# Performance work log

Measured on AMD Instinct MI355X. Metric: run time of the kernel, lower is better.

The kernel has to match this reference:

```python
import jax, jax.numpy as jnp
import numpy as np

BATCH_SIZE = 8388608            # arg_dict['batch_size']
REG_FACTORS = (0.01, 0.001)     # regular_factor_list
LOG_CLAMP = -100.0              # torch BCELoss clamps log outputs at -100


def setup_inputs() -> dict:
    key = jax.random.key(0)
    k1, k2, k3, k4 = jax.random.split(key, 4)
    B = BATCH_SIZE
    model_outputs = jax.random.uniform(k1, (B,), dtype=jnp.float32)
    labels = jax.random.uniform(k2, (B,), dtype=jnp.float32)
    # weight tensors of the regularized sub-modules (e.g. two Linear layers)
    w1 = jax.random.normal(k3, (4096, 4096), dtype=jnp.float32) * 0.02
    w2 = jax.random.normal(k4, (4096, 1024), dtype=jnp.float32) * 0.02
    return {"model_outputs": model_outputs, "labels": labels, "w1": w1, "w2": w2}


def reference(model_outputs, labels, w1, w2):
    p = model_outputs.reshape(labels.shape)
    # BCE with torch-style log clamping (log clamped to >= -100)
    log_p = jnp.clip(jnp.log(p), LOG_CLAMP)
    log_1mp = jnp.clip(jnp.log1p(-p), LOG_CLAMP)
    cross_loss = -jnp.mean(labels * log_p + (1.0 - labels) * log_1mp)
    # L2 regularization: sum(factor * ||w||^2 / (2 * batch_size))
    reg = (REG_FACTORS[0] * jnp.sum(w1 * w1) / (2.0 * BATCH_SIZE)
           + REG_FACTORS[1] * jnp.sum(w2 * w2) / (2.0 * BATCH_SIZE))
    result = cross_loss + reg
    # vectorized replacement of the per-sample python accuracy loop
    correct_count = jnp.sum(jnp.abs(p - labels) < 0.5)
    return result, correct_count
```

## Files before the change

### kernel.cpp

```cpp
#include <hip/hip_runtime.h>
#include <hip/hip_bf16.h>

#define GRID  2048
#define BLOCK 256
#define LOG_CLAMP -100.0f

struct Partials {
    float bce[GRID];
    float w1s[GRID];
    float w2s[GRID];
    unsigned int cnt[GRID];
};

__device__ __forceinline__ float wave_reduce_f(float v) {
#pragma unroll
    for (int o = 32; o > 0; o >>= 1) v += __shfl_down(v, o, 64);
    return v;
}
__device__ __forceinline__ unsigned int wave_reduce_u(unsigned int v) {
#pragma unroll
    for (int o = 32; o > 0; o >>= 1) v += __shfl_down(v, o, 64);
    return v;
}
__device__ __forceinline__ double wave_reduce_d(double v) {
#pragma unroll
    for (int o = 32; o > 0; o >>= 1) v += __shfl_down(v, o, 64);
    return v;
}

__device__ __forceinline__ float fast_ln(float x) {
    return __logf(x);
}

__global__ __launch_bounds__(BLOCK) void reduce_kernel(
    const float* __restrict__ p, const float* __restrict__ y,
    const float* __restrict__ w1, const float* __restrict__ w2,
    int nB4, int n14, int n24, Partials* __restrict__ ws)
{
    const float4* __restrict__ p4  = (const float4*)p;
    const float4* __restrict__ y4  = (const float4*)y;
    const float4* __restrict__ w14 = (const float4*)w1;
    const float4* __restrict__ w24 = (const float4*)w2;

    const int tid    = blockIdx.x * BLOCK + threadIdx.x;
    const int stride = GRID * BLOCK;

    float bce = 0.0f, s1 = 0.0f, s2 = 0.0f;
    unsigned int cnt = 0;

    for (int i = tid; i < nB4; i += stride) {
        float4 pv = p4[i];
        float4 yv = y4[i];
#define BCE_COMP(px, yx)                                                \
        {                                                               \
            float lp  = fmaxf(fast_ln(px), LOG_CLAMP);                  \
            float l1  = fmaxf(fast_ln(1.0f - (px)), LOG_CLAMP);         \
                               \
            bce += l1 + (yx) * (lp - l1);                               \
            cnt += (fabsf((px) - (yx)) < 0.5f) ? 1u : 0u;               \
        }
        BCE_COMP(pv.x, yv.x)
        BCE_COMP(pv.y, yv.y)
        BCE_COMP(pv.z, yv.z)
        BCE_COMP(pv.w, yv.w)
#undef BCE_COMP
    }

    for (int i = tid; i < n14; i += stride) {
        float4 v = w14[i];
        s1 += v.x * v.x + v.y * v.y + v.z * v.z + v.w * v.w;
    }

    for (int i = tid; i < n24; i += stride) {
        float4 v = w24[i];
        s2 += v.x * v.x + v.y * v.y + v.z * v.z + v.w * v.w;
    }

    float rb = wave_reduce_f(bce);
    float r1 = wave_reduce_f(s1);
    float r2 = wave_reduce_f(s2);
    unsigned int rc = wave_reduce_u(cnt);

    __shared__ float sb[BLOCK / 64], s1s[BLOCK / 64], s2s[BLOCK / 64];
    __shared__ unsigned int scs[BLOCK / 64];
    const int wave = threadIdx.x >> 6;
    const int lane = threadIdx.x & 63;
    if (lane == 0) { sb[wave] = rb; s1s[wave] = r1; s2s[wave] = r2; scs[wave] = rc; }
    __syncthreads();
    if (threadIdx.x == 0) {
        float tb = 0.0f, t1 = 0.0f, t2 = 0.0f;
        unsigned int tc = 0;
#pragma unroll
        for (int w = 0; w < BLOCK / 64; ++w) { tb += sb[w]; t1 += s1s[w]; t2 += s2s[w]; tc += scs[w]; }
        ws->bce[blockIdx.x] = tb;
        ws->w1s[blockIdx.x] = t1;
        ws->w2s[blockIdx.x] = t2;
        ws->cnt[blockIdx.x] = tc;
    }
}

__global__ __launch_bounds__(BLOCK) void finalize_kernel(
    const Partials* __restrict__ ws, float* __restrict__ out, int nB)
{
    double bce = 0.0, s1 = 0.0, s2 = 0.0;
    unsigned int cnt = 0;
    for (int i = threadIdx.x; i < GRID; i += BLOCK) {
        bce += (double)ws->bce[i];
        s1  += (double)ws->w1s[i];
        s2  += (double)ws->w2s[i];
        cnt += ws->cnt[i];
    }
    double rb = wave_reduce_d(bce);
    double r1 = wave_reduce_d(s1);
    double r2 = wave_reduce_d(s2);
    unsigned int rc = wave_reduce_u(cnt);

    __shared__ double sb[BLOCK / 64], s1s[BLOCK / 64], s2s[BLOCK / 64];
    __shared__ unsigned int scs[BLOCK / 64];
    const int wave = threadIdx.x >> 6;
    const int lane = threadIdx.x & 63;
    if (lane == 0) { sb[wave] = rb; s1s[wave] = r1; s2s[wave] = r2; scs[wave] = rc; }
    __syncthreads();
    if (threadIdx.x == 0) {
        double tb = 0.0, t1 = 0.0, t2 = 0.0;
        unsigned int tc = 0;
#pragma unroll
        for (int w = 0; w < BLOCK / 64; ++w) { tb += sb[w]; t1 += s1s[w]; t2 += s2s[w]; tc += scs[w]; }
        const double invB = 1.0 / (double)nB;
        double result = -tb * invB + (0.01 * t1 + 0.001 * t2) * (0.5 * invB);
        out[0] = (float)result;
        out[1] = (float)tc;
    }
}

extern "C" void kernel_launch(void* const* d_in, const int* in_sizes, int n_in,
                              void* d_out, int out_size, void* d_ws, size_t ws_size,
                              hipStream_t stream) {
    const float* p  = (const float*)d_in[0];
    const float* y  = (const float*)d_in[1];
    const float* w1 = (const float*)d_in[2];
    const float* w2 = (const float*)d_in[3];
    const int nB = in_sizes[0];
    const int n1 = in_sizes[2];
    const int n2 = in_sizes[3];

    Partials* ws = (Partials*)d_ws;
    float* out = (float*)d_out;

    reduce_kernel<<<GRID, BLOCK, 0, stream>>>(p, y, w1, w2, nB / 4, n1 / 4, n2 / 4, ws);
    finalize_kernel<<<1, BLOCK, 0, stream>>>(ws, out, nB);
}
```

Baseline: 165.3 us.

## Specialize reduction into one-shot blocks with fixed per-block tiles and tree finalize

For the known problem sizes, launches a large grid where each block handles a fixed tile of either the BCE data, w1, or w2, with several independent float4 loads per thread and no grid-stride loop. Per-block partials are pre-scaled and reduced by two small finalize kernels instead of one double-precision kernel. This aims to expose far more memory-level parallelism to approach HBM bandwidth, at the cost of size specialization, an extra launch, and float rather than double final accumulation.

```diff
diff --git a/kernel.cpp b/kernel.cpp
--- a/kernel.cpp
+++ b/kernel.cpp
@@ -1,15 +1,29 @@
 #include <hip/hip_runtime.h>
 #include <hip/hip_bf16.h>
 
-#define GRID  2048
 #define BLOCK 256
 #define LOG_CLAMP -100.0f
 
-struct Partials {
-    float bce[GRID];
-    float w1s[GRID];
-    float w2s[GRID];
-    unsigned int cnt[GRID];
+constexpr int NB = 8388608;
+constexpr int N1 = 4096 * 4096;
+constexpr int N2 = 4096 * 1024;
+
+constexpr int GROUPS = 1024;
+constexpr int NBLK_F = 9 * GROUPS;
+constexpr int S1_F   = NBLK_F / BLOCK;
+
+constexpr int GRID_G = 2048;
+constexpr int S1_G   = GRID_G / BLOCK;
+
+constexpr float SC_BCE = (float)(-1.0 / (double)NB);
+constexpr float SC_W1  = (float)(0.01 / (2.0 * (double)NB));
+constexpr float SC_W2  = (float)(0.001 / (2.0 * (double)NB));
+
+struct WS {
+    float        val[NBLK_F];
+    unsigned int cnt[NBLK_F];
+    float        s2v[64];
+    unsigned int s2c[64];
 };
 
 __device__ __forceinline__ float wave_reduce_f(float v) {
@@ -22,115 +36,162 @@
     for (int o = 32; o > 0; o >>= 1) v += __shfl_down(v, o, 64);
     return v;
 }
-__device__ __forceinline__ double wave_reduce_d(double v) {
-#pragma unroll
-    for (int o = 32; o > 0; o >>= 1) v += __shfl_down(v, o, 64);
-    return v;
-}
-
-__device__ __forceinline__ float fast_ln(float x) {
-    return __logf(x);
-}
-
-__global__ __launch_bounds__(BLOCK) void reduce_kernel(
+
+#define BCE_COMP(px, yx)                                            \
+    {                                                               \
+        float lp  = fmaxf(__logf(px), LOG_CLAMP);                   \
+        float l1  = fmaxf(__logf(1.0f - (px)), LOG_CLAMP);          \
+        acc += l1 + (yx) * (lp - l1);                               \
+        c   += (fabsf((px) - (yx)) < 0.5f) ? 1u : 0u;               \
+    }
+
+__device__ __forceinline__ float dot4(float4 v) {
+    return v.x * v.x + v.y * v.y + v.z * v.z + v.w * v.w;
+}
+
+__global__ __launch_bounds__(BLOCK) void reduce_split(
+    const float4* __restrict__ p4, const float4* __restrict__ y4,
+    const float4* __restrict__ w14, const float4* __restrict__ w24,
+    float* __restrict__ val, unsigned int* __restrict__ cnt)
+{
+    const int b = blockIdx.x;
+    const int g = b / 9;
+    const int r = b - g * 9;
+    const int t = threadIdx.x;
+
+    float acc = 0.0f;
+    unsigned int c = 0;
+    float scale;
+
+    if (r < 4) {
+        const int base = (g * 4 + r) * 512 + t;
+        float4 pa = p4[base];
+        float4 pb = p4[base + 256];
+        float4 ya = y4[base];
+        float4 yb = y4[base + 256];
+        BCE_COMP(pa.x, ya.x) BCE_COMP(pa.y, ya.y)
+        BCE_COMP(pa.z, ya.z) BCE_COMP(pa.w, ya.w)
+        BCE_COMP(pb.x, yb.x) BCE_COMP(pb.y, yb.y)
+        BCE_COMP(pb.z, yb.z) BCE_COMP(pb.w, yb.w)
+        scale = SC_BCE;
+    } else if (r < 8) {
+        const int base = (g * 4 + (r - 4)) * 1024 + t;
+        float4 a0 = w14[base];
+        float4 a1 = w14[base + 256];
+        float4 a2 = w14[base + 512];
+        float4 a3 = w14[base + 768];
+        acc = dot4(a0) + dot4(a1) + dot4(a2) + dot4(a3);
+        scale = SC_W1;
+    } else {
+        const int base = g * 1024 + t;
+        float4 b0 = w24[base];
+        float4 b1 = w24[base + 256];
+        float4 b2 = w24[base + 512];
+        float4 b3 = w24[base + 768];
+        acc = dot4(b0) + dot4(b1) + dot4(b2) + dot4(b3);
+        scale = SC_W2;
+    }
+
+    float rv = wave_reduce_f(acc);
+    unsigned int rc = wave_reduce_u(c);
+
+    __shared__ float sv[BLOCK / 64];
+    __shared__ unsigned int scn[BLOCK / 64];
+    const int wave = t >> 6;
+    const int lane = t & 63;
+    if (lane == 0) { sv[wave] = rv; scn[wave] = rc; }
+    __syncthreads();
+    if (t == 0) {
+        float tv = sv[0] + sv[1] + sv[2] + sv[3];
+        unsigned int tc = scn[0] + scn[1] + scn[2] + scn[3];
+        val[b] = tv * scale;
+        cnt[b] = tc;
+    }
+}
+
+__global__ __launch_bounds__(BLOCK) void reduce_generic(
     const float* __restrict__ p, const float* __restrict__ y,
     const float* __restrict__ w1, const float* __restrict__ w2,
-    int nB4, int n14, int n24, Partials* __restrict__ ws)
+    int nB4, int n14, int n24, int nB,
+    float* __restrict__ val, unsigned int* __restrict__ cnt)
 {
     const float4* __restrict__ p4  = (const float4*)p;
     const float4* __restrict__ y4  = (const float4*)y;
     const float4* __restrict__ w14 = (const float4*)w1;
     const float4* __restrict__ w24 = (const float4*)w2;
 
-    const int tid    = blockIdx.x * BLOCK + threadIdx.x;
-    const int stride = GRID * BLOCK;
-
-    float bce = 0.0f, s1 = 0.0f, s2 = 0.0f;
-    unsigned int cnt = 0;
+    const int tid = blockIdx.x * BLOCK + threadIdx.x;
+    const int stride = GRID_G * BLOCK;
+
+    float acc = 0.0f, s1 = 0.0f, s2 = 0.0f;
+    unsigned int c = 0;
 
     for (int i = tid; i < nB4; i += stride) {
         float4 pv = p4[i];
         float4 yv = y4[i];
-#define BCE_COMP(px, yx)                                                \
-        {                                                               \
-            float lp  = fmaxf(fast_ln(px), LOG_CLAMP);                  \
-            float l1  = fmaxf(fast_ln(1.0f - (px)), LOG_CLAMP);         \
-                               \
-            bce += l1 + (yx) * (lp - l1);                               \
-            cnt += (fabsf((px) - (yx)) < 0.5f) ? 1u : 0u;               \
-        }
-        BCE_COMP(pv.x, yv.x)
-        BCE_COMP(pv.y, yv.y)
-        BCE_COMP(pv.z, yv.z)
-        BCE_COMP(pv.w, yv.w)
-#undef BCE_COMP
-    }
-
-    for (int i = tid; i < n14; i += stride) {
-        float4 v = w14[i];
-        s1 += v.x * v.x + v.y * v.y + v.z * v.z + v.w * v.w;
-    }
-
-    for (int i = tid; i < n24; i += stride) {
-        float4 v = w24[i];
-        s2 += v.x * v.x + v.y * v.y + v.z * v.z + v.w * v.w;
-    }
-
-    float rb = wave_reduce_f(bce);
+        BCE_COMP(pv.x, yv.x) BCE_COMP(pv.y, yv.y)
+        BCE_COMP(pv.z, yv.z) BCE_COMP(pv.w, yv.w)
+    }
+    for (int i = tid; i < n14; i += stride) s1 += dot4(w14[i]);
+    for (int i = tid; i < n24; i += stride) s2 += dot4(w24[i]);
+
+    float rb = wave_reduce_f(acc);
     float r1 = wave_reduce_f(s1);
     float r2 = wave_reduce_f(s2);
-    unsigned int rc = wave_reduce_u(cnt);
+    unsigned int rc = wave_reduce_u(c);
 
     __shared__ float sb[BLOCK / 64], s1s[BLOCK / 64], s2s[BLOCK / 64];
-    __shared__ unsigned int scs[BLOCK / 64];
+    __shared__ unsigned int scn[BLOCK / 64];
     const int wave = threadIdx.x >> 6;
     const int lane = threadIdx.x & 63;
-    if (lane == 0) { sb[wave] = rb; s1s[wave] = r1; s2s[wave] = r2; scs[wave] = rc; }
-    __syncthreads();
-    if (threadIdx.x == 0) {
-        float tb = 0.0f, t1 = 0.0f, t2 = 0.0f;
-        unsigned int tc = 0;
-#pragma unroll
-        for (int w = 0; w < BLOCK / 64; ++w) { tb += sb[w]; t1 += s1s[w]; t2 += s2s[w]; tc += scs[w]; }
-        ws->bce[blockIdx.x] = tb;
-        ws->w1s[blockIdx.x] = t1;
-        ws->w2s[blockIdx.x] = t2;
-        ws->cnt[blockIdx.x] = tc;
-    }
-}
-
-__global__ __launch_bounds__(BLOCK) void finalize_kernel(
-    const Partials* __restrict__ ws, float* __restrict__ out, int nB)
-{
-    double bce = 0.0, s1 = 0.0, s2 = 0.0;
-    unsigned int cnt = 0;
-    for (int i = threadIdx.x; i < GRID; i += BLOCK) {
-        bce += (double)ws->bce[i];
-        s1  += (double)ws->w1s[i];
-        s2  += (double)ws->w2s[i];
-        cnt += ws->cnt[i];
-    }
-    double rb = wave_reduce_d(bce);
-    double r1 = wave_reduce_d(s1);
-    double r2 = wave_reduce_d(s2);
-    unsigned int rc = wave_reduce_u(cnt);
-
-    __shared__ double sb[BLOCK / 64], s1s[BLOCK / 64], s2s[BLOCK / 64];
-    __shared__ unsigned int scs[BLOCK / 64];
-    const int wave = threadIdx.x >> 6;
-    const int lane = threadIdx.x & 63;
-    if (lane == 0) { sb[wave] = rb; s1s[wave] = r1; s2s[wave] = r2; scs[wave] = rc; }
+    if (lane == 0) { sb[wave] = rb; s1s[wave] = r1; s2s[wave] = r2; scn[wave] = rc; }
     __syncthreads();
     if (threadIdx.x == 0) {
         double tb = 0.0, t1 = 0.0, t2 = 0.0;
         unsigned int tc = 0;
 #pragma unroll
-        for (int w = 0; w < BLOCK / 64; ++w) { tb += sb[w]; t1 += s1s[w]; t2 += s2s[w]; tc += scs[w]; }
+        for (int w = 0; w < BLOCK / 64; ++w) { tb += sb[w]; t1 += s1s[w]; t2 += s2s[w]; tc += scn[w]; }
         const double invB = 1.0 / (double)nB;
-        double result = -tb * invB + (0.01 * t1 + 0.001 * t2) * (0.5 * invB);
-        out[0] = (float)result;
-        out[1] = (float)tc;
-    }
+        val[blockIdx.x] = (float)(-tb * invB + (0.01 * t1 + 0.001 * t2) * (0.5 * invB));
+        cnt[blockIdx.x] = tc;
+    }
+}
+
+__global__ __launch_bounds__(BLOCK) void finalize1(
+    const float* __restrict__ val, const unsigned int* __restrict__ cnt, int n,
+    float* __restrict__ s2v, unsigned int* __restrict__ s2c)
+{
+    const int i = blockIdx.x * BLOCK + threadIdx.x;
+    float v = (i < n) ? val[i] : 0.0f;
+    unsigned int c = (i < n) ? cnt[i] : 0u;
+
+    float rv = wave_reduce_f(v);
+    unsigned int rc = wave_reduce_u(c);
+
+    __shared__ float sv[BLOCK / 64];
+    __shared__ unsigned int scn[BLOCK / 64];
+    const int wave = threadIdx.x >> 6;
+    const int lane = threadIdx.x & 63;
+    if (lane == 0) { sv[wave] = rv; scn[wave] = rc; }
+    __syncthreads();
+    if (threadIdx.x == 0) {
+        float tv = sv[0] + sv[1] + sv[2] + sv[3];
+        unsigned int tc = scn[0] + scn[1] + scn[2] + scn[3];
+        s2v[blockIdx.x] = tv;
+        s2c[blockIdx.x] = tc;
+    }
+}
+
+__global__ void finalize2(
+    const float* __restrict__ s2v, const unsigned int* __restrict__ s2c,
+    int n, float* __restrict__ out)
+{
+    const int t = threadIdx.x;
+    float v = (t < n) ? s2v[t] : 0.0f;
+    unsigned int c = (t < n) ? s2c[t] : 0u;
+    v = wave_reduce_f(v);
+    c = wave_reduce_u(c);
+    if (t == 0) { out[0] = v; out[1] = (float)c; }
 }
 
 extern "C" void kernel_launch(void* const* d_in, const int* in_sizes, int n_in,
@@ -144,9 +205,19 @@
     const int n1 = in_sizes[2];
     const int n2 = in_sizes[3];
 
-    Partials* ws = (Partials*)d_ws;
+    WS* ws = (WS*)d_ws;
     float* out = (float*)d_out;
 
-    reduce_kernel<<<GRID, BLOCK, 0, stream>>>(p, y, w1, w2, nB / 4, n1 / 4, n2 / 4, ws);
-    finalize_kernel<<<1, BLOCK, 0, stream>>>(ws, out, nB);
-}
+    if (nB == NB && n1 == N1 && n2 == N2 && in_sizes[1] == NB) {
+        reduce_split<<<NBLK_F, BLOCK, 0, stream>>>(
+            (const float4*)p, (const float4*)y, (const float4*)w1, (const float4*)w2,
+            ws->val, ws->cnt);
+        finalize1<<<S1_F, BLOCK, 0, stream>>>(ws->val, ws->cnt, NBLK_F, ws->s2v, ws->s2c);
+        finalize2<<<1, 64, 0, stream>>>(ws->s2v, ws->s2c, S1_F, out);
+    } else {
+        reduce_generic<<<GRID_G, BLOCK, 0, stream>>>(
+            p, y, w1, w2, nB / 4, n1 / 4, n2 / 4, nB, ws->val, ws->cnt);
+        finalize1<<<S1_G, BLOCK, 0, stream>>>(ws->val, ws->cnt, GRID_G, ws->s2v, ws->s2c);
+        finalize2<<<1, 64, 0, stream>>>(ws->s2v, ws->s2c, S1_G, out);
+    }
+}
```

Result: no change. 165.4 us (+0.1%).
